# Performance work log

Hardware: AMD Instinct MI355X
Metric: run time of the kernel (lower is better)

## Reference

```python
import jax, jax.numpy as jnp
import numpy as np

DIM = 1024
HEADS = 16
SCALE = DIM ** -0.5  # NOTE: original scales by full dim, not head dim


def setup_inputs() -> dict:
    key = jax.random.key(0)
    ks = jax.random.split(key, 6)
    B, S, D = 2, 2048, DIM
    x = jax.random.normal(ks[0], (B, S, D), dtype=jnp.float32)
    Wq = jax.random.normal(ks[1], (D, D), dtype=jnp.float32) * 0.02
    Wk = jax.random.normal(ks[2], (D, D), dtype=jnp.float32) * 0.02
    Wv = jax.random.normal(ks[3], (D, D), dtype=jnp.float32) * 0.02
    Wo = jax.random.normal(ks[4], (D, D), dtype=jnp.float32) * 0.02
    z = jnp.zeros((D,), dtype=jnp.float32)
    return {"x": x, "Wq": Wq, "bq": z, "Wk": Wk, "bk": z, "Wv": Wv, "bv": z, "Wo": Wo, "bo": z}


def reference(x, Wq, bq, Wk, bk, Wv, bv, Wo, bo):
    B, S, D = x.shape
    H = HEADS
    d = D // H
    # projections (Linear: x @ W + b)
    q = (x @ Wq + bq).reshape(B, S, H, d).transpose(0, 2, 1, 3)  # b h i d
    k = (x @ Wk + bk).reshape(B, S, H, d).transpose(0, 2, 1, 3)  # b h j d
    v = (x @ Wv + bv).reshape(B, S, H, d).transpose(0, 2, 1, 3)  # b h j d
    dots = jnp.einsum("bhid,bhjd->bhij", q, k) * SCALE
    # causal mask: strict upper triangle -> -inf
    mask = jnp.triu(jnp.ones((S, S), dtype=bool), k=1)
    dots = jnp.where(mask, -jnp.inf, dots)
    attn = jax.nn.softmax(dots, axis=-1)
    out = jnp.einsum("bhij,bhjd->bhid", attn, v)
    out = out.transpose(0, 2, 1, 3).reshape(B, S, D)  # b i (h d)
    return out @ Wo + bo
```

## Files before the change

### kernel.cpp

```cpp
#include <hip/hip_runtime.h>
#include <hip/hip_bf16.h>

typedef __bf16 bf16;
typedef __bf16 bf16x4 __attribute__((ext_vector_type(4)));
typedef __bf16 bf16x8 __attribute__((ext_vector_type(8)));
typedef float floatx4 __attribute__((ext_vector_type(4)));

#define MFMA_16x16x32(a, b, c) __builtin_amdgcn_mfma_f32_16x16x32_bf16((a), (b), (c), 0, 0, 0)
#define NEG_INF (-__builtin_inff())

#define CB 2
#define CS 2048
#define CD 1024
#define CH 16
#define CM (CB * CS)
#define QSC (0.03125f * 1.44269504088896340736f)

__device__ __forceinline__ void async16(const bf16* g, bf16* l) {
    __builtin_amdgcn_global_load_lds(
        (const __attribute__((address_space(1))) void*)g,
        (__attribute__((address_space(3))) void*)l, 16, 0, 0);
}

__global__ __launch_bounds__(256) void prep(
    const float* __restrict__ x, bf16* __restrict__ xb,
    const float* __restrict__ W0, const float* __restrict__ W1,
    const float* __restrict__ W2, const float* __restrict__ W3,
    bf16* __restrict__ Wt) {
    __shared__ bf16 Ws[64 * 68];
    const int t = threadIdx.x;
    if (blockIdx.x < 2048) {
        size_t i = ((size_t)blockIdx.x * 256 + t) * 8;
        float4 a = *(const float4*)(x + i);
        float4 b = *(const float4*)(x + i + 4);
        bf16x8 v;
        v[0] = (bf16)a.x; v[1] = (bf16)a.y; v[2] = (bf16)a.z; v[3] = (bf16)a.w;
        v[4] = (bf16)b.x; v[5] = (bf16)b.y; v[6] = (bf16)b.z; v[7] = (bf16)b.w;
        *(bf16x8*)(xb + i) = v;
        return;
    }
    const int bid = blockIdx.x - 2048;
    const int z = bid >> 8, rem = bid & 255;
    const int k0 = (rem >> 4) * 64, n0 = (rem & 15) * 64;
    const float* W = z == 0 ? W0 : z == 1 ? W1 : z == 2 ? W2 : W3;
    bf16* out = Wt + (size_t)z * CD * CD;
    const int rr = t >> 4, c4 = (t & 15) * 4;
#pragma unroll
    for (int i = 0; i < 4; i++) {
        int r = rr + i * 16;
        float4 f = *(const float4*)(W + (size_t)(k0 + r) * CD + n0 + c4);
        bf16x4 v;
        v[0] = (bf16)f.x; v[1] = (bf16)f.y; v[2] = (bf16)f.z; v[3] = (bf16)f.w;
        *(bf16x4*)&Ws[r * 68 + c4] = v;
    }
    __syncthreads();
#pragma unroll
    for (int i = 0; i < 4; i++) {
        int n = rr + i * 16;
        bf16x4 v;
#pragma unroll
        for (int j = 0; j < 4; j++) v[j] = Ws[(c4 + j) * 68 + n];
        *(bf16x4*)(out + (size_t)(n0 + n) * CD + k0 + c4) = v;
    }
}

__global__ __launch_bounds__(256) void gemm_qkv(
    const bf16* __restrict__ A, const bf16* __restrict__ Bt,
    const float* __restrict__ bq, const float* __restrict__ bk,
    const float* __restrict__ bv,
    bf16* __restrict__ Qb, bf16* __restrict__ Kb, bf16* __restrict__ Vb) {
    __shared__ bf16 As[128 * 32];
    __shared__ bf16 Bs[128 * 32];
    const int t = threadIdx.x, w = t >> 6, lane = t & 63;
    const int quad = lane >> 4, l15 = lane & 15;
    const int which = blockIdx.x >> 3;
    const int bn = (blockIdx.x & 7) * 128, bm = blockIdx.y * 128;
    const bf16* Bw = Bt + (size_t)which * CD * CD;

    const bf16* ag = A + (size_t)(bm + w * 16 + (lane >> 2)) * CD + (lane & 3) * 8;
    const bf16* bg = Bw + (size_t)(bn + w * 16 + (lane >> 2)) * CD + (lane & 3) * 8;
    const int lo = w * 16 * 32;

    const int wm = (w >> 1) * 64, wn = (w & 1) * 64;
    floatx4 acc[4][4] = {};

    for (int k0 = 0; k0 < CD; k0 += 32) {
        async16(ag + k0, &As[lo]);
        async16(ag + (size_t)64 * CD + k0, &As[lo + 64 * 32]);
        async16(bg + k0, &Bs[lo]);
        async16(bg + (size_t)64 * CD + k0, &Bs[lo + 64 * 32]);
        __syncthreads();
        bf16x8 af[4], bfr[4];
#pragma unroll
        for (int mt = 0; mt < 4; mt++)
            af[mt] = *(const bf16x8*)&As[(wm + mt * 16 + l15) * 32 + quad * 8];
#pragma unroll
        for (int nt = 0; nt < 4; nt++)
            bfr[nt] = *(const bf16x8*)&Bs[(wn + nt * 16 + l15) * 32 + quad * 8];
#pragma unroll
        for (int mt = 0; mt < 4; mt++)
#pragma unroll
            for (int nt = 0; nt < 4; nt++)
                acc[mt][nt] = MFMA_16x16x32(af[mt], bfr[nt], acc[mt][nt]);
        __syncthreads();
    }

    const float* bias = which == 0 ? bq : which == 1 ? bk : bv;
    bf16* out = which == 0 ? Qb : Kb;
#pragma unroll
    for (int mt = 0; mt < 4; mt++) {
#pragma unroll
        for (int nt = 0; nt < 4; nt++) {
            int token = bm + wm + mt * 16 + quad * 4;
            int col = bn + wn + nt * 16 + l15;
            int b = token >> 11, s = token & (CS - 1);
            int h = col >> 6, dd = col & 63;
            if (which == 2) {
                bf16x4 pv;
#pragma unroll
                for (int r = 0; r < 4; r++) pv[r] = (bf16)(acc[mt][nt][r] + bias[col]);
                *(bf16x4*)&Vb[(((size_t)(b * CH + h)) * 64 + dd) * CS + s] = pv;
            } else {
#pragma unroll
                for (int r = 0; r < 4; r++) {
                    float v = acc[mt][nt][r] + bias[col];
                    if (which == 0) v *= QSC;
                    out[(((size_t)(b * CH + h)) * CS + s + r) * 64 + dd] = (bf16)v;
                }
            }
        }
    }
}

__global__ __launch_bounds__(256) void gemm_o(
    const bf16* __restrict__ A, const bf16* __restrict__ Bt,
    const float* __restrict__ bias, float* __restrict__ out) {
    __shared__ bf16 As[128 * 32];
    __shared__ bf16 Bs[128 * 32];
    const int t = threadIdx.x, w = t >> 6, lane = t & 63;
    const int quad = lane >> 4, l15 = lane & 15;
    const int bn = blockIdx.x * 128, bm = blockIdx.y * 128;

    const bf16* ag = A + (size_t)(bm + w * 16 + (lane >> 2)) * CD + (lane & 3) * 8;
    const bf16* bg = Bt + (size_t)(bn + w * 16 + (lane >> 2)) * CD + (lane & 3) * 8;
    const int lo = w * 16 * 32;

    const int wm = (w >> 1) * 64, wn = (w & 1) * 64;
    floatx4 acc[4][4] = {};

    for (int k0 = 0; k0 < CD; k0 += 32) {
        async16(ag + k0, &As[lo]);
        async16(ag + (size_t)64 * CD + k0, &As[lo + 64 * 32]);
        async16(bg + k0, &Bs[lo]);
        async16(bg + (size_t)64 * CD + k0, &Bs[lo + 64 * 32]);
        __syncthreads();
        bf16x8 af[4], bfr[4];
#pragma unroll
        for (int mt = 0; mt < 4; mt++)
            af[mt] = *(const bf16x8*)&As[(wm + mt * 16 + l15) * 32 + quad * 8];
#pragma unroll
        for (int nt = 0; nt < 4; nt++)
            bfr[nt] = *(const bf16x8*)&Bs[(wn + nt * 16 + l15) * 32 + quad * 8];
#pragma unroll
        for (int mt = 0; mt < 4; mt++)
#pragma unroll
            for (int nt = 0; nt < 4; nt++)
                acc[mt][nt] = MFMA_16x16x32(af[mt], bfr[nt], acc[mt][nt]);
        __syncthreads();
    }

#pragma unroll
    for (int mt = 0; mt < 4; mt++)
#pragma unroll
        for (int nt = 0; nt < 4; nt++)
#pragma unroll
            for (int r = 0; r < 4; r++) {
                int row = bm + wm + mt * 16 + quad * 4 + r;
                int col = bn + wn + nt * 16 + l15;
                out[(size_t)row * CD + col] = acc[mt][nt][r] + bias[col];
            }
}

__global__ __launch_bounds__(512) void attn_kernel(
    const bf16* __restrict__ Q, const bf16* __restrict__ Kg,
    const bf16* __restrict__ Vg, bf16* __restrict__ Ob) {
    __shared__ bf16 Ks[2][2][64 * 72];
    __shared__ bf16 Vt[2][2][64 * 72];
    __shared__ bf16 Pt[8][32 * 72];

    const int t = threadIdx.x;
    const int w = t >> 6, lane = t & 63;
    const int grp = w >> 2, wg = w & 3;
    const int quad = lane >> 4, l15 = lane & 15;

    const int qb = 15 - (blockIdx.x >> 5);
    const int bh = blockIdx.x & 31;
    const int q0 = qb * 128;
    const int wrow0 = q0 + wg * 32;
    const int nT = 2 * qb + 2;
    const int nS = nT >> 1;

    const bf16* Qh = Q + (size_t)bh * CS * 64;
    const bf16* Kh = Kg + (size_t)bh * CS * 64;
    const bf16* Vh = Vg + (size_t)bh * 64 * CS;

    const int tl = t & 255;
    const int strow = tl >> 2, soff = (tl & 3) * 16;
    const bf16* ksrc = Kh + (size_t)strow * 64 + soff;
    const bf16* vsrc = Vh + (size_t)strow * CS + soff;
    const int sbase = strow * 72 + soff;

    {
        const bf16* k0p = ksrc + (size_t)grp * 64 * 64;
        const bf16* v0p = vsrc + grp * 64;
        bf16x8 a = *(const bf16x8*)k0p, b = *(const bf16x8*)(k0p + 8);
        bf16x8 c = *(const bf16x8*)v0p, d = *(const bf16x8*)(v0p + 8);
        *(bf16x8*)&Ks[grp][0][sbase]     = a;
        *(bf16x8*)&Ks[grp][0][sbase + 8] = b;
        *(bf16x8*)&Vt[grp][0][sbase]     = c;
        *(bf16x8*)&Vt[grp][0][sbase + 8] = d;
    }
    bf16x8 kr0, kr1, vr0, vr1;
    {
        int t1 = (grp + 2 < nT) ? grp + 2 : 0;
        const bf16* kn = ksrc + (size_t)t1 * 64 * 64;
        const bf16* vn = vsrc + t1 * 64;
        kr0 = *(const bf16x8*)kn;  kr1 = *(const bf16x8*)(kn + 8);
        vr0 = *(const bf16x8*)vn;  vr1 = *(const bf16x8*)(vn + 8);
    }

    bf16x8 qf[2][2];
#pragma unroll
    for (int g = 0; g < 2; g++) {
        const bf16* qsrc = Qh + (size_t)(wrow0 + g * 16 + l15) * 64 + quad * 8;
        qf[g][0] = *(const bf16x8*)qsrc;
        qf[g][1] = *(const bf16x8*)(qsrc + 32);
    }

    floatx4 o[4][2] = {};
    float m_r[2] = {NEG_INF, NEG_INF};
    float l_r[2] = {0.f, 0.f};

    bf16* pw = Pt[w];

    for (int s = 0; s < nS; s++) {
        const int tile = 2 * s + grp;
        const int cur = s & 1;
        const int ks0 = tile * 64;
        __syncthreads();

        *(bf16x8*)&Ks[grp][cur ^ 1][sbase]     = kr0;
        *(bf16x8*)&Ks[grp][cur ^ 1][sbase + 8] = kr1;
        *(bf16x8*)&Vt[grp][cur ^ 1][sbase]     = vr0;
        *(bf16x8*)&Vt[grp][cur ^ 1][sbase + 8] = vr1;
        {
            int nk = (tile + 4 < nT) ? tile + 4 : 0;
            const bf16* kn = ksrc + (size_t)nk * 64 * 64;
            const bf16* vn = vsrc + nk * 64;
            kr0 = *(const bf16x8*)kn;  kr1 = *(const bf16x8*)(kn + 8);
            vr0 = *(const bf16x8*)vn;  vr1 = *(const bf16x8*)(vn + 8);
        }
        if (ks0 > wrow0 + 31) continue;

        const bf16* ksb = Ks[grp][cur];
        const bf16* vtb = Vt[grp][cur];

        floatx4 sc[2][4] = {};
        __builtin_amdgcn_s_setprio(1);
#pragma unroll
        for (int nt = 0; nt < 4; nt++) {
            bf16x8 af0 = *(const bf16x8*)&ksb[(nt * 16 + l15) * 72 + quad * 8];
            bf16x8 af1 = *(const bf16x8*)&ksb[(nt * 16 + l15) * 72 + 32 + quad * 8];
#pragma unroll
            for (int g = 0; g < 2; g++) {
                sc[g][nt] = MFMA_16x16x32(af0, qf[g][0], sc[g][nt]);
                sc[g][nt] = MFMA_16x16x32(af1, qf[g][1], sc[g][nt]);
            }
        }
        __builtin_amdgcn_s_setprio(0);
        if (ks0 + 63 > wrow0) {
#pragma unroll
            for (int g = 0; g < 2; g++) {
                int qrow = wrow0 + g * 16 + l15;
#pragma unroll
                for (int nt = 0; nt < 4; nt++)
#pragma unroll
                    for (int r = 0; r < 4; r++)
                        if (ks0 + nt * 16 + quad * 4 + r > qrow)
                            sc[g][nt][r] = NEG_INF;
            }
        }
        float mx[2];
#pragma unroll
        for (int g = 0; g < 2; g++) {
            floatx4 v01, v23, vm;
#pragma unroll
            for (int c = 0; c < 4; c++) {
                v01[c] = fmaxf(sc[g][0][c], sc[g][1][c]);
                v23[c] = fmaxf(sc[g][2][c], sc[g][3][c]);
                vm[c] = fmaxf(v01[c], v23[c]);
            }
            float m = fmaxf(fmaxf(vm[0], vm[1]), fmaxf(vm[2], vm[3]));
            m = fmaxf(m, __shfl_xor(m, 16));
            m = fmaxf(m, __shfl_xor(m, 32));
            mx[g] = m;
        }
        int need = (mx[0] > m_r[0] + 8.f) || (mx[1] > m_r[1] + 8.f);
        if (__any(need)) {
#pragma unroll
            for (int g = 0; g < 2; g++) {
                float mn = fmaxf(m_r[g], mx[g]);
                float a = __builtin_amdgcn_exp2f(m_r[g] - mn);
                m_r[g] = mn;
                l_r[g] *= a;
#pragma unroll
                for (int dt = 0; dt < 4; dt++)
#pragma unroll
                    for (int r = 0; r < 4; r++) o[dt][g][r] *= a;
            }
        }
#pragma unroll
        for (int g = 0; g < 2; g++) {
#pragma unroll
            for (int nt = 0; nt < 4; nt++)
#pragma unroll
                for (int r = 0; r < 4; r++)
                    sc[g][nt][r] = __builtin_amdgcn_exp2f(sc[g][nt][r] - m_r[g]);
            floatx4 st = (sc[g][0] + sc[g][1]) + (sc[g][2] + sc[g][3]);
            l_r[g] += (st[0] + st[1]) + (st[2] + st[3]);
        }
#pragma unroll
        for (int g = 0; g < 2; g++)
#pragma unroll
            for (int nt = 0; nt < 4; nt++) {
                bf16x4 pk;
#pragma unroll
                for (int r = 0; r < 4; r++) pk[r] = (bf16)sc[g][nt][r];
                *(bf16x4*)&pw[(g * 16 + l15) * 72 + nt * 16 + quad * 4] = pk;
            }
        bf16x8 bp[2][2];
#pragma unroll
        for (int g = 0; g < 2; g++) {
            bp[g][0] = *(const bf16x8*)&pw[(g * 16 + l15) * 72 + quad * 8];
            bp[g][1] = *(const bf16x8*)&pw[(g * 16 + l15) * 72 + 32 + quad * 8];
        }
        __builtin_amdgcn_s_setprio(1);
#pragma unroll
        for (int dt = 0; dt < 4; dt++) {
            bf16x8 av0 = *(const bf16x8*)&vtb[(dt * 16 + l15) * 72 + quad * 8];
            bf16x8 av1 = *(const bf16x8*)&vtb[(dt * 16 + l15) * 72 + 32 + quad * 8];
#pragma unroll
            for (int g = 0; g < 2; g++) {
                o[dt][g] = MFMA_16x16x32(av0, bp[g][0], o[dt][g]);
                o[dt][g] = MFMA_16x16x32(av1, bp[g][1], o[dt][g]);
            }
        }
        __builtin_amdgcn_s_setprio(0);
    }

    __syncthreads();
    float* mg = (float*)&Ks[0][0][0];
    float* base = mg + (size_t)(wg * 64 + lane) * 36;
    if (grp == 1) {
#pragma unroll
        for (int dt = 0; dt < 4; dt++)
#pragma unroll
            for (int g = 0; g < 2; g++)
                *(floatx4*)(base + (dt * 2 + g) * 4) = o[dt][g];
        base[32] = m_r[0]; base[33] = m_r[1];
        base[34] = l_r[0]; base[35] = l_r[1];
    }
    __syncthreads();
    if (grp == 0) {
        float a0[2], a1[2];
#pragma unroll
        for (int g = 0; g < 2; g++) {
            float m1 = base[32 + g], l1 = base[34 + g];
            float mm = fmaxf(m_r[g], m1);
            a0[g] = __builtin_amdgcn_exp2f(m_r[g] - mm);
            a1[g] = __builtin_amdgcn_exp2f(m1 - mm);
            l_r[g] = l_r[g] * a0[g] + l1 * a1[g];
        }
#pragma unroll
        for (int dt = 0; dt < 4; dt++)
#pragma unroll
            for (int g = 0; g < 2; g++) {
                floatx4 o1 = *(const floatx4*)(base + (dt * 2 + g) * 4);
#pragma unroll
                for (int r = 0; r < 4; r++)
                    o[dt][g][r] = o[dt][g][r] * a0[g] + o1[r] * a1[g];
            }
        const int b = bh >> 4, h = bh & 15;
#pragma unroll
        for (int g = 0; g < 2; g++) {
            float l = l_r[g];
            l += __shfl_xor(l, 16);
            l += __shfl_xor(l, 32);
            float rl = 1.f / l;
            int row = wrow0 + g * 16 + l15;
#pragma unroll
            for (int dt = 0; dt < 4; dt++) {
                bf16x4 ov;
#pragma unroll
                for (int r = 0; r < 4; r++) ov[r] = (bf16)(o[dt][g][r] * rl);
                *(bf16x4*)&Ob[((size_t)b * CS + row) * CD + h * 64 + dt * 16 + quad * 4] = ov;
            }
        }
    }
}

extern "C" void kernel_launch(void* const* d_in, const int* in_sizes, int n_in,
                              void* d_out, int out_size, void* d_ws, size_t ws_size,
                              hipStream_t stream) {
    const float* x  = (const float*)d_in[0];
    const float* Wq = (const float*)d_in[1];
    const float* bq = (const float*)d_in[2];
    const float* Wk = (const float*)d_in[3];
    const float* bk = (const float*)d_in[4];
    const float* Wv = (const float*)d_in[5];
    const float* bv = (const float*)d_in[6];
    const float* Wo = (const float*)d_in[7];
    const float* bo = (const float*)d_in[8];
    float* out = (float*)d_out;

    bf16* xb = (bf16*)d_ws;
    bf16* Wt = xb + (size_t)CM * CD;
    bf16* Qb = Wt + (size_t)4 * CD * CD;
    bf16* Kb = Qb + (size_t)CB * CH * CS * 64;
    bf16* Vb = Kb + (size_t)CB * CH * CS * 64;
    bf16* Ob = Vb + (size_t)CB * CH * CS * 64;

    prep<<<3072, 256, 0, stream>>>(x, xb, Wq, Wk, Wv, Wo, Wt);

    gemm_qkv<<<dim3(24, CM / 128), 256, 0, stream>>>(
        xb, Wt, bq, bk, bv, Qb, Kb, Vb);

    attn_kernel<<<512, 512, 0, stream>>>(Qb, Kb, Vb, Ob);

    gemm_o<<<dim3(8, CM / 128), 256, 0, stream>>>(
        Ob, Wt + (size_t)3 * CD * CD, bo, out);
}
```

Baseline: 187.3 us.

## Feed P directly from registers via 16x16x16 MFMA and reorder query-block scheduling

Removes the per-wave LDS round trip for the softmax probabilities. The score accumulator layout is converted to bf16 and used directly as the B operand of 16x16x16 bf16 MFMAs, with V^T fragments read as 4-element slices. This drops LDS stores and loads plus the Pt buffer, which frees shared memory, but it doubles the MFMA instruction count and uses narrower LDS reads. The block-index mapping is also changed so blocks 256+ take query blocks in ascending order, while the first 256 keep the descending heavy-first order.

```diff
diff --git a/kernel.cpp b/kernel.cpp
--- a/kernel.cpp
+++ b/kernel.cpp
@@ -5,8 +5,10 @@
 typedef __bf16 bf16x4 __attribute__((ext_vector_type(4)));
 typedef __bf16 bf16x8 __attribute__((ext_vector_type(8)));
 typedef float floatx4 __attribute__((ext_vector_type(4)));
+typedef short shortx4 __attribute__((ext_vector_type(4)));
 
 #define MFMA_16x16x32(a, b, c) __builtin_amdgcn_mfma_f32_16x16x32_bf16((a), (b), (c), 0, 0, 0)
+#define MFMA_16x16x16(a, b, c) __builtin_amdgcn_mfma_f32_16x16x16bf16_1k((a), (b), (c), 0, 0, 0)
 #define NEG_INF (-__builtin_inff())
 
 #define CB 2
@@ -20,6 +22,12 @@
     __builtin_amdgcn_global_load_lds(
         (const __attribute__((address_space(1))) void*)g,
         (__attribute__((address_space(3))) void*)l, 16, 0, 0);
+}
+
+__device__ __forceinline__ shortx4 to_s4(floatx4 v) {
+    bf16x4 b;
+    b[0] = (bf16)v[0]; b[1] = (bf16)v[1]; b[2] = (bf16)v[2]; b[3] = (bf16)v[3];
+    return __builtin_bit_cast(shortx4, b);
 }
 
 __global__ __launch_bounds__(256) void prep(
@@ -186,15 +194,15 @@
     const bf16* __restrict__ Vg, bf16* __restrict__ Ob) {
     __shared__ bf16 Ks[2][2][64 * 72];
     __shared__ bf16 Vt[2][2][64 * 72];
-    __shared__ bf16 Pt[8][32 * 72];
 
     const int t = threadIdx.x;
     const int w = t >> 6, lane = t & 63;
     const int grp = w >> 2, wg = w & 3;
     const int quad = lane >> 4, l15 = lane & 15;
 
-    const int qb = 15 - (blockIdx.x >> 5);
-    const int bh = blockIdx.x & 31;
+    const int bid = blockIdx.x;
+    const int qb = bid < 256 ? 15 - (bid >> 5) : (bid - 256) >> 5;
+    const int bh = bid & 31;
     const int q0 = qb * 128;
     const int wrow0 = q0 + wg * 32;
     const int nT = 2 * qb + 2;
@@ -240,8 +248,6 @@
     floatx4 o[4][2] = {};
     float m_r[2] = {NEG_INF, NEG_INF};
     float l_r[2] = {0.f, 0.f};
-
-    bf16* pw = Pt[w];
 
     for (int s = 0; s < nS; s++) {
         const int tile = 2 * s + grp;
@@ -329,31 +335,24 @@
             floatx4 st = (sc[g][0] + sc[g][1]) + (sc[g][2] + sc[g][3]);
             l_r[g] += (st[0] + st[1]) + (st[2] + st[3]);
         }
+        shortx4 pb[2][4];
 #pragma unroll
         for (int g = 0; g < 2; g++)
 #pragma unroll
-            for (int nt = 0; nt < 4; nt++) {
-                bf16x4 pk;
-#pragma unroll
-                for (int r = 0; r < 4; r++) pk[r] = (bf16)sc[g][nt][r];
-                *(bf16x4*)&pw[(g * 16 + l15) * 72 + nt * 16 + quad * 4] = pk;
-            }
-        bf16x8 bp[2][2];
-#pragma unroll
-        for (int g = 0; g < 2; g++) {
-            bp[g][0] = *(const bf16x8*)&pw[(g * 16 + l15) * 72 + quad * 8];
-            bp[g][1] = *(const bf16x8*)&pw[(g * 16 + l15) * 72 + 32 + quad * 8];
-        }
+            for (int nt = 0; nt < 4; nt++) pb[g][nt] = to_s4(sc[g][nt]);
         __builtin_amdgcn_s_setprio(1);
 #pragma unroll
-        for (int dt = 0; dt < 4; dt++) {
-            bf16x8 av0 = *(const bf16x8*)&vtb[(dt * 16 + l15) * 72 + quad * 8];
-            bf16x8 av1 = *(const bf16x8*)&vtb[(dt * 16 + l15) * 72 + 32 + quad * 8];
-#pragma unroll
-            for (int g = 0; g < 2; g++) {
-                o[dt][g] = MFMA_16x16x32(av0, bp[g][0], o[dt][g]);
-                o[dt][g] = MFMA_16x16x32(av1, bp[g][1], o[dt][g]);
-            }
+        for (int nt = 0; nt < 4; nt++) {
+            shortx4 av[4];
+#pragma unroll
+            for (int dt = 0; dt < 4; dt++)
+                av[dt] = __builtin_bit_cast(shortx4,
+                    *(const bf16x4*)&vtb[(dt * 16 + l15) * 72 + nt * 16 + quad * 4]);
+#pragma unroll
+            for (int dt = 0; dt < 4; dt++)
+#pragma unroll
+                for (int g = 0; g < 2; g++)
+                    o[dt][g] = MFMA_16x16x16(av[dt], pb[g][nt], o[dt][g]);
         }
         __builtin_amdgcn_s_setprio(0);
     }
```

After: 196.2 us. 1.05x slower.
